# Optimization experiments

Measured on AMD Instinct MI355X. Metric: run time of the kernel, lower is better.

Reference implementation:

```python
import jax, jax.numpy as jnp
import numpy as np

N = 20000   # nodes
E = 320000  # edges (before self-loops)
D = 256     # feature width (inChl = hdChl = outChl)
H = 4       # heads
C = D // H  # per-head channels = 64
NEG_SLOPE = 0.2
LN_EPS = 1e-5


def setup_inputs() -> dict:
    key = jax.random.key(0)
    ks = jax.random.split(key, 2 + 4 * 4)
    inp = {}
    inp["x"] = jax.random.normal(ks[0], (1, N, D), dtype=jnp.float32)
    inp["edge_index"] = jax.random.randint(ks[1], (2, E), 0, N, dtype=jnp.int32)
    s = 1.0 / np.sqrt(D)
    for i in range(4):
        k = 2 + 4 * i
        inp[f"Wl{i+1}"] = (jax.random.normal(ks[k], (D, H * C), dtype=jnp.float32) * s)
        inp[f"Wr{i+1}"] = (jax.random.normal(ks[k + 1], (D, H * C), dtype=jnp.float32) * s)
        inp[f"att{i+1}"] = (jax.random.normal(ks[k + 2], (H, C), dtype=jnp.float32) * s)
        inp[f"b{i+1}"] = jnp.zeros((H * C,), dtype=jnp.float32)
        inp[f"g{i+1}"] = jnp.ones((D,), dtype=jnp.float32)
        inp[f"be{i+1}"] = jnp.zeros((D,), dtype=jnp.float32)
    return inp


def _segment_softmax(scores, seg, num_segments):
    # scores: [E, H], per-destination softmax over incoming edges
    m = jax.ops.segment_max(scores, seg, num_segments=num_segments)
    e = jnp.exp(scores - m[seg])
    d = jax.ops.segment_sum(e, seg, num_segments=num_segments)
    return e / d[seg]


def _gatv2(x, src, dst, Wl, Wr, att, b):
    # GATv2Conv defaults: share_weights=False, concat=True, negative_slope=0.2
    n = x.shape[0]
    xl = (x @ Wl).reshape(n, H, C)  # source transform
    xr = (x @ Wr).reshape(n, H, C)  # target transform
    m = xl[src] + xr[dst]                                  # [E', H, C]
    e = jnp.sum(jax.nn.leaky_relu(m, NEG_SLOPE) * att, -1) # [E', H]
    alpha = _segment_softmax(e, dst, n)                    # [E', H]
    out = jax.ops.segment_sum(xl[src] * alpha[:, :, None], dst, num_segments=n)
    return out.reshape(n, H * C) + b


def _layernorm(x, g, b):
    mu = jnp.mean(x, -1, keepdims=True)
    var = jnp.mean(jnp.square(x - mu), -1, keepdims=True)
    return (x - mu) * jax.lax.rsqrt(var + LN_EPS) * g + b


def _forward(x, edge_index, layers):
    h = x[0]  # squeeze batch dim -> [N, D]
    n = h.shape[0]
    loop = jnp.arange(n, dtype=edge_index.dtype)
    src = jnp.concatenate([edge_index[0], loop])  # add_self_loops=True
    dst = jnp.concatenate([edge_index[1], loop])
    for (Wl, Wr, att, b, g, be) in layers:
        h = _gatv2(h, src, dst, Wl, Wr, att, b)
        h = jax.nn.relu(_layernorm(h, g, be))
    return h[None]  # unsqueeze -> [1, N, D]


def reference(x, edge_index,
              Wl1, Wr1, att1, b1, g1, be1,
              Wl2, Wr2, att2, b2, g2, be2,
              Wl3, Wr3, att3, b3, g3, be3,
              Wl4, Wr4, att4, b4, g4, be4):
    layers = [(Wl1, Wr1, att1, b1, g1, be1),
              (Wl2, Wr2, att2, b2, g2, be2),
              (Wl3, Wr3, att3, b3, g3, be3),
              (Wl4, Wr4, att4, b4, g4, be4)]
    return _forward(x, edge_index, layers)
```

## Files before the change

kernel.cpp:

```cpp
#include <hip/hip_runtime.h>
#include <math.h>

#define N_NODES 20000
#define E_EDGES 320000
#define EP (E_EDGES + N_NODES)
#define D 256
#define NHEAD 4
#define CH 64
#define NEG_SLOPE 0.2f
#define LN_EPS 1e-5f

typedef _Float16 half8_t __attribute__((ext_vector_type(8)));
typedef _Float16 half4_t __attribute__((ext_vector_type(4)));
typedef _Float16 half2_t __attribute__((ext_vector_type(2)));
typedef float   float4_t __attribute__((ext_vector_type(4)));

__device__ __forceinline__ void async_cp16(const void* g, void* l)
{
    __builtin_amdgcn_global_load_lds(
        (const __attribute__((address_space(1))) void*)g,
        (__attribute__((address_space(3))) void*)l, 16, 0, 0);
}

__global__ __launch_bounds__(256)
void convert_x_kernel(const float* __restrict__ x, _Float16* __restrict__ h16,
                      int* __restrict__ deg)
{
    int i = blockIdx.x * 256 + threadIdx.x;
    if (i < N_NODES) deg[i] = 0;
    if (i >= N_NODES * D / 4) return;
    float4 v = reinterpret_cast<const float4*>(x)[i];
    half4_t o;
    o.x = (_Float16)v.x; o.y = (_Float16)v.y; o.z = (_Float16)v.z; o.w = (_Float16)v.w;
    reinterpret_cast<half4_t*>(h16)[i] = o;
}

__global__ __launch_bounds__(256)
void csr_hist_kernel(const int* __restrict__ ei, int* __restrict__ deg)
{
    int e = blockIdx.x * 256 + threadIdx.x;
    if (e >= EP) return;
    int dst = (e < E_EDGES) ? ei[E_EDGES + e] : (e - E_EDGES);
    atomicAdd(&deg[dst], 1);
}

__global__ __launch_bounds__(1024)
void csr_scan_kernel(const int* __restrict__ deg, int* __restrict__ rowptr,
                     int* __restrict__ cursor)
{
    __shared__ int wsum[16];
    int t = threadIdx.x, lane = t & 63, w = t >> 6;
    int base = t * 20;
    int loc[20];
    int s = 0;
    #pragma unroll
    for (int k = 0; k < 20; ++k) {
        int idx = base + k;
        loc[k] = (idx < N_NODES) ? deg[idx] : 0;
        s += loc[k];
    }
    int x = s;
    #pragma unroll
    for (int o = 1; o < 64; o <<= 1) {
        int y = __shfl_up(x, o, 64);
        if (lane >= o) x += y;
    }
    if (lane == 63) wsum[w] = x;
    __syncthreads();
    if (t == 0) {
        int sacc = 0;
        #pragma unroll
        for (int k = 0; k < 16; ++k) { int tmp = wsum[k]; wsum[k] = sacc; sacc += tmp; }
        rowptr[N_NODES] = sacc;
    }
    __syncthreads();
    int excl = wsum[w] + x - s;
    #pragma unroll
    for (int k = 0; k < 20; ++k) {
        int idx = base + k;
        if (idx < N_NODES) { rowptr[idx] = excl; cursor[idx] = excl; }
        excl += loc[k];
    }
}

__global__ __launch_bounds__(256)
void csr_scatter_kernel(const int* __restrict__ ei, int* __restrict__ cursor,
                        int* __restrict__ csr_src)
{
    int e = blockIdx.x * 256 + threadIdx.x;
    if (e >= EP) return;
    int src, dst;
    if (e < E_EDGES) { src = ei[e]; dst = ei[E_EDGES + e]; }
    else             { src = dst = e - E_EDGES; }
    int pos = atomicAdd(&cursor[dst], 1);
    csr_src[pos] = src;
}

struct WPtrs { const float* p[8]; };
__global__ __launch_bounds__(256)
void convw_all_kernel(WPtrs wp, _Float16* __restrict__ Wt_all)
{
    __shared__ float tile[64][65];
    const float* W = wp.p[blockIdx.z];
    _Float16* out = Wt_all + (size_t)blockIdx.z * 65536;
    int bx = blockIdx.x * 64, by = blockIdx.y * 64;
    int t = threadIdx.x;
    #pragma unroll
    for (int i = 0; i < 16; ++i) {
        int idx = t + i * 256;
        int kk = idx >> 6, nn = idx & 63;
        tile[kk][nn] = W[(by + kk) * 256 + bx + nn];
    }
    __syncthreads();
    #pragma unroll
    for (int i = 0; i < 16; ++i) {
        int idx = t + i * 256;
        int nn = idx >> 6, kk = idx & 63;
        out[(bx + nn) * 256 + by + kk] = (_Float16)tile[kk][nn];
    }
}

#define BM 128
#define BN 128
#define BK 64
#define EPAD 136
__global__ __launch_bounds__(256)
void gemm_f16_kernel(const _Float16* __restrict__ A16, const _Float16* __restrict__ Wt,
                     _Float16* __restrict__ X0, _Float16* __restrict__ X1, int nrows)
{
    const _Float16* W = Wt + blockIdx.z * 65536 + blockIdx.y * (BN * 256);
    _Float16* X = blockIdx.z ? X1 : X0;
    const int row0 = blockIdx.x * BM;
    const int col0 = blockIdx.y * BN;

    __shared__ __align__(1024) char smem[4 * 32 * EPAD * 2];
    _Float16 (*As)[BK] = reinterpret_cast<_Float16 (*)[BK]>(smem);
    _Float16 (*Bs)[BK] = reinterpret_cast<_Float16 (*)[BK]>(smem + BM * BK * 2);
    _Float16* As_flat = reinterpret_cast<_Float16*>(smem);
    _Float16* Bs_flat = reinterpret_cast<_Float16*>(smem + BM * BK * 2);
    _Float16* ep = reinterpret_cast<_Float16*>(smem);

    const int tid  = threadIdx.x;
    const int wave = tid >> 6, lane = tid & 63;
    const int quad = lane >> 4, l16 = lane & 15;

    float4_t acc[2][8];
    #pragma unroll
    for (int i = 0; i < 2; ++i)
        #pragma unroll
        for (int j = 0; j < 8; ++j) acc[i][j] = (float4_t)0.0f;

    const int r_in  = lane >> 3;
    const int c_in  = (lane & 7) * 8;

    #pragma unroll
    for (int k0 = 0; k0 < 256; k0 += BK) {
        #pragma unroll
        for (int j = 0; j < 4; ++j) {
            int ia  = wave * 4 + j;
            int row = ia * 8 + r_in;
            int gra = row0 + row;
            gra = (gra < nrows) ? gra : (nrows - 1);
            async_cp16(A16 + (size_t)gra * 256 + k0 + c_in, As_flat + ia * 512);
            async_cp16(W   + (size_t)row * 256 + k0 + c_in, Bs_flat + ia * 512);
        }
        __syncthreads();

        #pragma unroll
        for (int s = 0; s < 2; ++s) {
            half8_t af[2], bf[8];
            #pragma unroll
            for (int i = 0; i < 2; ++i)
                af[i] = *reinterpret_cast<const half8_t*>(&As[wave * 32 + i * 16 + l16][s * 32 + quad * 8]);
            #pragma unroll
            for (int j = 0; j < 8; ++j)
                bf[j] = *reinterpret_cast<const half8_t*>(&Bs[j * 16 + l16][s * 32 + quad * 8]);
            #pragma unroll
            for (int i = 0; i < 2; ++i)
                #pragma unroll
                for (int j = 0; j < 8; ++j)
                    acc[i][j] = __builtin_amdgcn_mfma_f32_16x16x32_f16(af[i], bf[j], acc[i][j], 0, 0, 0);
        }
        __syncthreads();
    }

    _Float16* epw = ep + wave * 32 * EPAD;
    #pragma unroll
    for (int i = 0; i < 2; ++i)
        #pragma unroll
        for (int j = 0; j < 8; ++j)
            #pragma unroll
            for (int r = 0; r < 4; ++r)
                epw[(i * 16 + quad * 4 + r) * EPAD + j * 16 + l16] = (_Float16)acc[i][j][r];
    #pragma unroll
    for (int t = 0; t < 8; ++t) {
        int row = t * 4 + quad;
        int gr = row0 + wave * 32 + row;
        half8_t v = *reinterpret_cast<const half8_t*>(&epw[row * EPAD + l16 * 8]);
        if (gr < nrows)
            *reinterpret_cast<half8_t*>(X + gr * 256 + col0 + l16 * 8) = v;
    }
}

__global__ __launch_bounds__(256)
void gat_fused_kernel(const _Float16* __restrict__ xl, const _Float16* __restrict__ xr,
                      const int* __restrict__ rowptr, const int* __restrict__ csr_src,
                      const float* __restrict__ att,
                      const float* __restrict__ bias, const float* __restrict__ g,
                      const float* __restrict__ be,
                      float* __restrict__ out32, _Float16* __restrict__ out16,
                      int write32)
{
    const int tid = threadIdx.x;
    const int w = tid >> 6, lane = tid & 63;
    const int n = blockIdx.x * 4 + w;
    const int start = rowptr[n], end = rowptr[n + 1];
    const int c0 = lane * 4;

    half2_t xr01, xr23, att01, att23;
    {
        half4_t xh = *reinterpret_cast<const half4_t*>(xr + n * D + c0);
        xr01.x = xh.x; xr01.y = xh.y; xr23.x = xh.z; xr23.y = xh.w;
        float4 av = *reinterpret_cast<const float4*>(att + c0);
        att01.x = (_Float16)av.x; att01.y = (_Float16)av.y;
        att23.x = (_Float16)av.z; att23.y = (_Float16)av.w;
    }
    const half2_t k02 = {(_Float16)NEG_SLOPE, (_Float16)NEG_SLOPE};

    float den = 0.0f;
    float4 num = make_float4(0.0f, 0.0f, 0.0f, 0.0f);

    int i = start;
    for (; i + 2 <= end; i += 2) {
        int s0 = csr_src[i];
        int s1 = csr_src[i + 1];
        half4_t ha = *reinterpret_cast<const half4_t*>(xl + s0 * D + c0);
        half4_t hb = *reinterpret_cast<const half4_t*>(xl + s1 * D + c0);

        half2_t a01 = {ha.x, ha.y}, a23 = {ha.z, ha.w};
        half2_t b01 = {hb.x, hb.y}, b23 = {hb.z, hb.w};
        half2_t t0 = a01 + xr01, t1 = a23 + xr23;
        half2_t u0 = b01 + xr01, u1 = b23 + xr23;
        t0 = __builtin_elementwise_max(t0, t0 * k02);
        t1 = __builtin_elementwise_max(t1, t1 * k02);
        u0 = __builtin_elementwise_max(u0, u0 * k02);
        u1 = __builtin_elementwise_max(u1, u1 * k02);
        float va = __builtin_amdgcn_fdot2(t0, att01, 0.0f, false);
        va       = __builtin_amdgcn_fdot2(t1, att23, va,   false);
        float vb = __builtin_amdgcn_fdot2(u0, att01, 0.0f, false);
        vb       = __builtin_amdgcn_fdot2(u1, att23, vb,   false);
        #pragma unroll
        for (int o = 1; o < 16; o <<= 1) {
            va += __shfl_xor(va, o, 64);
            vb += __shfl_xor(vb, o, 64);
        }
        float pa = __expf(va), pb = __expf(vb);
        den += pa + pb;
        num.x = fmaf(pa, (float)ha.x, num.x); num.x = fmaf(pb, (float)hb.x, num.x);
        num.y = fmaf(pa, (float)ha.y, num.y); num.y = fmaf(pb, (float)hb.y, num.y);
        num.z = fmaf(pa, (float)ha.z, num.z); num.z = fmaf(pb, (float)hb.z, num.z);
        num.w = fmaf(pa, (float)ha.w, num.w); num.w = fmaf(pb, (float)hb.w, num.w);
    }
    if (i < end) {
        int s0 = csr_src[i];
        half4_t ha = *reinterpret_cast<const half4_t*>(xl + s0 * D + c0);
        half2_t a01 = {ha.x, ha.y}, a23 = {ha.z, ha.w};
        half2_t t0 = a01 + xr01, t1 = a23 + xr23;
        t0 = __builtin_elementwise_max(t0, t0 * k02);
        t1 = __builtin_elementwise_max(t1, t1 * k02);
        float va = __builtin_amdgcn_fdot2(t0, att01, 0.0f, false);
        va       = __builtin_amdgcn_fdot2(t1, att23, va,   false);
        #pragma unroll
        for (int o = 1; o < 16; o <<= 1) va += __shfl_xor(va, o, 64);
        float pa = __expf(va);
        den += pa;
        num.x = fmaf(pa, (float)ha.x, num.x);
        num.y = fmaf(pa, (float)ha.y, num.y);
        num.z = fmaf(pa, (float)ha.z, num.z);
        num.w = fmaf(pa, (float)ha.w, num.w);
    }

    float inv_den = 1.0f / den;
    float4 bi = *reinterpret_cast<const float4*>(bias + c0);
    float a0 = fmaf(num.x, inv_den, bi.x);
    float a1 = fmaf(num.y, inv_den, bi.y);
    float a2 = fmaf(num.z, inv_den, bi.z);
    float a3 = fmaf(num.w, inv_den, bi.w);

    float wsum = a0 + a1 + a2 + a3;
    float wsq  = a0 * a0 + a1 * a1 + a2 * a2 + a3 * a3;
    #pragma unroll
    for (int o = 1; o < 64; o <<= 1) {
        wsum += __shfl_xor(wsum, o, 64);
        wsq  += __shfl_xor(wsq,  o, 64);
    }
    float mu = wsum * (1.0f / 256.0f);
    float var = wsq * (1.0f / 256.0f) - mu * mu;
    float rstd = rsqrtf(var + LN_EPS);

    float4 gg = *reinterpret_cast<const float4*>(g + c0);
    float4 bb = *reinterpret_cast<const float4*>(be + c0);
    float o0 = fmaxf((a0 - mu) * rstd * gg.x + bb.x, 0.0f);
    float o1 = fmaxf((a1 - mu) * rstd * gg.y + bb.y, 0.0f);
    float o2 = fmaxf((a2 - mu) * rstd * gg.z + bb.z, 0.0f);
    float o3 = fmaxf((a3 - mu) * rstd * gg.w + bb.w, 0.0f);

    if (write32) {
        float4 o4 = make_float4(o0, o1, o2, o3);
        *reinterpret_cast<float4*>(out32 + n * D + c0) = o4;
    } else {
        half4_t o4;
        o4.x = (_Float16)o0; o4.y = (_Float16)o1; o4.z = (_Float16)o2; o4.w = (_Float16)o3;
        *reinterpret_cast<half4_t*>(out16 + n * D + c0) = o4;
    }
}

extern "C" void kernel_launch(void* const* d_in, const int* in_sizes, int n_in,
                              void* d_out, int out_size, void* d_ws, size_t ws_size,
                              hipStream_t stream)
{
    const float* x  = (const float*)d_in[0];
    const int*   ei = (const int*)d_in[1];

    char* ws = (char*)d_ws;
    size_t off = 0;
    _Float16* h16   = (_Float16*)(ws + off); off += (size_t)N_NODES * D * 2;
    _Float16* xl    = (_Float16*)(ws + off); off += (size_t)N_NODES * D * 2;
    _Float16* xr    = (_Float16*)(ws + off); off += (size_t)N_NODES * D * 2;
    _Float16* WtA   = (_Float16*)(ws + off); off += (size_t)8 * 65536 * 2;
    int* rowptr     = (int*)(ws + off);      off += (size_t)(N_NODES + 32) * 4;
    int* cursor     = (int*)(ws + off);      off += (size_t)N_NODES * 4;
    int* csr_src    = (int*)(ws + off);      off += (size_t)EP * 4;

    convert_x_kernel<<<(N_NODES * D / 4 + 255) / 256, 256, 0, stream>>>(x, h16, cursor);
    csr_hist_kernel<<<(EP + 255) / 256, 256, 0, stream>>>(ei, cursor);
    csr_scan_kernel<<<1, 1024, 0, stream>>>(cursor, rowptr, cursor);
    csr_scatter_kernel<<<(EP + 255) / 256, 256, 0, stream>>>(ei, cursor, csr_src);

    WPtrs wp;
    for (int l = 0; l < 4; ++l) {
        wp.p[2 * l + 0] = (const float*)d_in[2 + 6 * l + 0];
        wp.p[2 * l + 1] = (const float*)d_in[2 + 6 * l + 1];
    }
    convw_all_kernel<<<dim3(4, 4, 8), 256, 0, stream>>>(wp, WtA);

    dim3 gemm_grid((N_NODES + BM - 1) / BM, 256 / BN, 2);

    for (int l = 0; l < 4; ++l) {
        const float* att  = (const float*)d_in[2 + 6 * l + 2];
        const float* bias = (const float*)d_in[2 + 6 * l + 3];
        const float* g    = (const float*)d_in[2 + 6 * l + 4];
        const float* be   = (const float*)d_in[2 + 6 * l + 5];

        gemm_f16_kernel<<<gemm_grid, 256, 0, stream>>>(h16, WtA + (size_t)l * 131072,
                                                       xl, xr, N_NODES);
        gat_fused_kernel<<<N_NODES / 4, 256, 0, stream>>>(xl, xr, rowptr, csr_src, att,
                                                          bias, g, be,
                                                          (float*)d_out, h16, (l == 3) ? 1 : 0);
    }
}
```

Before: 386.3 us.

## Unroll edge aggregation by eight and use DPP row reductions for scores

```diff
diff --git a/kernel.cpp b/kernel.cpp
--- a/kernel.cpp
+++ b/kernel.cpp
@@ -22,6 +22,19 @@
         (__attribute__((address_space(3))) void*)l, 16, 0, 0);
 }
 
+template<int CTRL>
+__device__ __forceinline__ float dpp_add(float v) {
+    int t = __builtin_amdgcn_update_dpp(0, __float_as_int(v), CTRL, 0xF, 0xF, true);
+    return v + __int_as_float(t);
+}
+__device__ __forceinline__ float row_sum16(float v) {
+    v = dpp_add<0x121>(v);
+    v = dpp_add<0x122>(v);
+    v = dpp_add<0x124>(v);
+    v = dpp_add<0x128>(v);
+    return v;
+}
+
 __global__ __launch_bounds__(256)
 void convert_x_kernel(const float* __restrict__ x, _Float16* __restrict__ h16,
                       int* __restrict__ deg)
@@ -46,10 +59,11 @@
 
 __global__ __launch_bounds__(1024)
 void csr_scan_kernel(const int* __restrict__ deg, int* __restrict__ rowptr,
-                     int* __restrict__ cursor)
+                     int* __restrict__ cursor, int* __restrict__ csr_src)
 {
     __shared__ int wsum[16];
     int t = threadIdx.x, lane = t & 63, w = t >> 6;
+    if (t < 8) csr_src[EP + t] = 0;
     int base = t * 20;
     int loc[20];
     int s = 0;
@@ -231,53 +245,66 @@
     float4 num = make_float4(0.0f, 0.0f, 0.0f, 0.0f);
 
     int i = start;
-    for (; i + 2 <= end; i += 2) {
-        int s0 = csr_src[i];
-        int s1 = csr_src[i + 1];
-        half4_t ha = *reinterpret_cast<const half4_t*>(xl + s0 * D + c0);
-        half4_t hb = *reinterpret_cast<const half4_t*>(xl + s1 * D + c0);
-
-        half2_t a01 = {ha.x, ha.y}, a23 = {ha.z, ha.w};
-        half2_t b01 = {hb.x, hb.y}, b23 = {hb.z, hb.w};
-        half2_t t0 = a01 + xr01, t1 = a23 + xr23;
-        half2_t u0 = b01 + xr01, u1 = b23 + xr23;
-        t0 = __builtin_elementwise_max(t0, t0 * k02);
-        t1 = __builtin_elementwise_max(t1, t1 * k02);
-        u0 = __builtin_elementwise_max(u0, u0 * k02);
-        u1 = __builtin_elementwise_max(u1, u1 * k02);
-        float va = __builtin_amdgcn_fdot2(t0, att01, 0.0f, false);
-        va       = __builtin_amdgcn_fdot2(t1, att23, va,   false);
-        float vb = __builtin_amdgcn_fdot2(u0, att01, 0.0f, false);
-        vb       = __builtin_amdgcn_fdot2(u1, att23, vb,   false);
-        #pragma unroll
-        for (int o = 1; o < 16; o <<= 1) {
-            va += __shfl_xor(va, o, 64);
-            vb += __shfl_xor(vb, o, 64);
-        }
-        float pa = __expf(va), pb = __expf(vb);
-        den += pa + pb;
-        num.x = fmaf(pa, (float)ha.x, num.x); num.x = fmaf(pb, (float)hb.x, num.x);
-        num.y = fmaf(pa, (float)ha.y, num.y); num.y = fmaf(pb, (float)hb.y, num.y);
-        num.z = fmaf(pa, (float)ha.z, num.z); num.z = fmaf(pb, (float)hb.z, num.z);
-        num.w = fmaf(pa, (float)ha.w, num.w); num.w = fmaf(pb, (float)hb.w, num.w);
-    }
-    if (i < end) {
-        int s0 = csr_src[i];
-        half4_t ha = *reinterpret_cast<const half4_t*>(xl + s0 * D + c0);
-        half2_t a01 = {ha.x, ha.y}, a23 = {ha.z, ha.w};
-        half2_t t0 = a01 + xr01, t1 = a23 + xr23;
-        t0 = __builtin_elementwise_max(t0, t0 * k02);
-        t1 = __builtin_elementwise_max(t1, t1 * k02);
-        float va = __builtin_amdgcn_fdot2(t0, att01, 0.0f, false);
-        va       = __builtin_amdgcn_fdot2(t1, att23, va,   false);
-        #pragma unroll
-        for (int o = 1; o < 16; o <<= 1) va += __shfl_xor(va, o, 64);
-        float pa = __expf(va);
-        den += pa;
-        num.x = fmaf(pa, (float)ha.x, num.x);
-        num.y = fmaf(pa, (float)ha.y, num.y);
-        num.z = fmaf(pa, (float)ha.z, num.z);
-        num.w = fmaf(pa, (float)ha.w, num.w);
+    for (; i + 8 <= end; i += 8) {
+        int sidx[8];
+        #pragma unroll
+        for (int j = 0; j < 8; ++j) sidx[j] = csr_src[i + j];
+        half4_t h[8];
+        #pragma unroll
+        for (int j = 0; j < 8; ++j)
+            h[j] = *reinterpret_cast<const half4_t*>(xl + sidx[j] * D + c0);
+        float p[8];
+        #pragma unroll
+        for (int j = 0; j < 8; ++j) {
+            half2_t a01 = {h[j].x, h[j].y}, a23 = {h[j].z, h[j].w};
+            half2_t t0 = a01 + xr01, t1 = a23 + xr23;
+            t0 = __builtin_elementwise_max(t0, t0 * k02);
+            t1 = __builtin_elementwise_max(t1, t1 * k02);
+            float v = __builtin_amdgcn_fdot2(t0, att01, 0.0f, false);
+            p[j]    = __builtin_amdgcn_fdot2(t1, att23, v,   false);
+        }
+        #pragma unroll
+        for (int j = 0; j < 8; ++j) p[j] = row_sum16(p[j]);
+        #pragma unroll
+        for (int j = 0; j < 8; ++j) p[j] = __expf(p[j]);
+        #pragma unroll
+        for (int j = 0; j < 8; ++j) {
+            den += p[j];
+            num.x = fmaf(p[j], (float)h[j].x, num.x);
+            num.y = fmaf(p[j], (float)h[j].y, num.y);
+            num.z = fmaf(p[j], (float)h[j].z, num.z);
+            num.w = fmaf(p[j], (float)h[j].w, num.w);
+        }
+    }
+    for (; i < end; i += 4) {
+        int sidx[4];
+        #pragma unroll
+        for (int j = 0; j < 4; ++j) sidx[j] = csr_src[i + j];
+        half4_t h[4];
+        #pragma unroll
+        for (int j = 0; j < 4; ++j)
+            h[j] = *reinterpret_cast<const half4_t*>(xl + sidx[j] * D + c0);
+        float p[4];
+        #pragma unroll
+        for (int j = 0; j < 4; ++j) {
+            half2_t a01 = {h[j].x, h[j].y}, a23 = {h[j].z, h[j].w};
+            half2_t t0 = a01 + xr01, t1 = a23 + xr23;
+            t0 = __builtin_elementwise_max(t0, t0 * k02);
+            t1 = __builtin_elementwise_max(t1, t1 * k02);
+            float v = __builtin_amdgcn_fdot2(t0, att01, 0.0f, false);
+            p[j]    = __builtin_amdgcn_fdot2(t1, att23, v,   false);
+        }
+        #pragma unroll
+        for (int j = 0; j < 4; ++j) p[j] = row_sum16(p[j]);
+        #pragma unroll
+        for (int j = 0; j < 4; ++j) {
+            float pj = (i + j < end) ? __expf(p[j]) : 0.0f;
+            den += pj;
+            num.x = fmaf(pj, (float)h[j].x, num.x);
+            num.y = fmaf(pj, (float)h[j].y, num.y);
+            num.z = fmaf(pj, (float)h[j].z, num.z);
+            num.w = fmaf(pj, (float)h[j].w, num.w);
+        }
     }
 
     float inv_den = 1.0f / den;
@@ -330,11 +357,11 @@
     _Float16* WtA   = (_Float16*)(ws + off); off += (size_t)8 * 65536 * 2;
     int* rowptr     = (int*)(ws + off);      off += (size_t)(N_NODES + 32) * 4;
     int* cursor     = (int*)(ws + off);      off += (size_t)N_NODES * 4;
-    int* csr_src    = (int*)(ws + off);      off += (size_t)EP * 4;
+    int* csr_src    = (int*)(ws + off);      off += (size_t)(EP + 32) * 4;
 
     convert_x_kernel<<<(N_NODES * D / 4 + 255) / 256, 256, 0, stream>>>(x, h16, cursor);
     csr_hist_kernel<<<(EP + 255) / 256, 256, 0, stream>>>(ei, cursor);
-    csr_scan_kernel<<<1, 1024, 0, stream>>>(cursor, rowptr, cursor);
+    csr_scan_kernel<<<1, 1024, 0, stream>>>(cursor, rowptr, cursor, csr_src);
     csr_scatter_kernel<<<(EP + 255) / 256, 256, 0, stream>>>(ei, cursor, csr_src);
 
     WPtrs wp;
```

Result: faster. 355.6 us (-7.9%).
